# Kernel tuning notes

Hardware: AMD Instinct MI355X
Metric: run time of the kernel (lower is better)

## Reference

```python
import jax, jax.numpy as jnp
import numpy as np

N_DST = 100_000
N_SRC = 200_000
DEG = 16            # fixed avg degree -> E = N_DST*DEG
E = N_DST * DEG
P, K, W = 16, 256, 8  # num_parts, codebook entries, part width; feat_dim = P*W = 128
F_IN = P * W
F_OUT = 128


def setup_inputs() -> dict:
    key = jax.random.key(0)
    k1, k2, k3, k4, k5, k6, k7 = jax.random.split(key, 7)
    codes = jax.random.randint(k1, (N_SRC, P), 0, K, dtype=jnp.int32)
    indices = jax.random.randint(k2, (E,), 0, N_SRC, dtype=jnp.int32)
    indptr = (jnp.arange(N_DST + 1, dtype=jnp.int32) * DEG)
    h_self = jax.random.normal(k3, (N_DST, F_IN), dtype=jnp.float32)
    codebook = jax.random.normal(k4, (P, K, W), dtype=jnp.float32)
    W_neigh = jax.random.normal(k5, (F_OUT, F_IN), dtype=jnp.float32) * (1.0 / np.sqrt(F_IN))
    W_self = jax.random.normal(k6, (F_OUT, F_IN), dtype=jnp.float32) * (1.0 / np.sqrt(F_IN))
    b_self = jax.random.normal(k7, (F_OUT,), dtype=jnp.float32) * 0.01
    return {"codes": codes, "indices": indices, "indptr": indptr, "h_self": h_self,
            "codebook": codebook, "W_neigh": W_neigh, "W_self": W_self, "b_self": b_self}


def reference(codes, indices, indptr, h_self, codebook, W_neigh, W_self, b_self):
    n_dst = indptr.shape[0] - 1
    n_edges = indices.shape[0]
    # --- VQ decompress: codebook[p, codes[n, p]] -> [N_src, P, W] -> [N_src, F_IN]
    feat = codebook[jnp.arange(P)[None, :], codes]          # [N_src, P, W]
    feat = feat.reshape(feat.shape[0], F_IN)                # [N_src, F_IN]
    # --- CSR(CSC) mean SpMM over neighbors
    # dst id of each edge from indptr (jit-safe, static E)
    dst_ids = jnp.searchsorted(indptr, jnp.arange(n_edges, dtype=indptr.dtype), side="right") - 1
    gathered = feat[indices]                                 # [E, F_IN] (irregular gather)
    summed = jax.ops.segment_sum(gathered, dst_ids, num_segments=n_dst)  # [N_dst, F_IN]
    deg = jnp.diff(indptr).astype(summed.dtype)
    h_neigh = summed / jnp.maximum(deg, 1.0)[:, None]        # mean aggregation
    # --- linear combine: fc_neigh(h_neigh) + fc_self(h_self)
    rst = h_neigh @ W_neigh.T + h_self @ W_self.T + b_self[None, :]
    return rst
```

## Files before the change

### kernel.cpp

```cpp
#include <hip/hip_runtime.h>
#include <stdint.h>

constexpr int N_DST = 100000;
constexpr int N_SRC = 200000;
constexpr int DEG   = 16;
constexpr int PP    = 16;
constexpr int KK    = 256;
constexpr int WW    = 8;
constexpr int F_IN  = 128;
constexpr int F_OUT = 128;

constexpr int DT = 64;
constexpr int NT = (N_DST + DT - 1) / DT;
constexpr int LDS_STRIDE = 264;
constexpr int NBLK = 256;

typedef __attribute__((ext_vector_type(8))) short short8;
typedef __attribute__((ext_vector_type(4))) float floatx4;

__device__ __forceinline__ unsigned short f2bf(float f) {
    unsigned int u = __float_as_uint(f);
    unsigned int r = (u + 0x7FFFu + ((u >> 16) & 1u)) >> 16;
    return (unsigned short)r;
}
__device__ __forceinline__ float bf2f(unsigned int bits16) {
    return __uint_as_float(bits16 << 16);
}

__device__ __forceinline__ void gather_loads(
    int d0, int tid, const int* __restrict__ indices,
    const int* __restrict__ codes, const float* __restrict__ h_self,
    int* c, float4* hv)
{
    const int lane = tid & 63;
    const int wv   = tid >> 6;
    const int p    = lane & 15;
    const int sub  = lane >> 4;
    const int d    = d0 + wv * 4 + sub;
    const int dd   = (d < N_DST) ? d : (N_DST - 1);

    int s[16];
    #pragma unroll
    for (int e = 0; e < 16; ++e) s[e] = indices[dd * DEG + e];

    #pragma unroll
    for (int it = 0; it < 2; ++it) {
        const int j  = tid + it * 1024;
        const int dl = j >> 5, kq = j & 31;
        const int dh = d0 + dl;
        hv[it] = make_float4(0.f, 0.f, 0.f, 0.f);
        if (dh < N_DST) hv[it] = ((const float4*)h_self)[(size_t)dh * 32 + kq];
    }

    #pragma unroll
    for (int e = 0; e < 16; ++e) c[e] = codes[s[e] * PP + p];
}

__device__ __forceinline__ void gather_finish(
    int tid, const int* c, const float4* hv,
    const unsigned short* __restrict__ scb,
    unsigned short (*buf)[LDS_STRIDE])
{
    const int lane = tid & 63;
    const int wv   = tid >> 6;
    const int p    = lane & 15;
    const int sub  = lane >> 4;

    float ga[8];
    #pragma unroll
    for (int i = 0; i < 8; ++i) ga[i] = 0.f;
    #pragma unroll
    for (int e = 0; e < 16; ++e) {
        const uint4 q = *(const uint4*)(scb + (((p << 8) | c[e]) << 3));
        ga[0] += bf2f(q.x & 0xFFFFu);
        ga[1] += bf2f(q.x >> 16);
        ga[2] += bf2f(q.y & 0xFFFFu);
        ga[3] += bf2f(q.y >> 16);
        ga[4] += bf2f(q.z & 0xFFFFu);
        ga[5] += bf2f(q.z >> 16);
        ga[6] += bf2f(q.w & 0xFFFFu);
        ga[7] += bf2f(q.w >> 16);
    }

    uint4 o4;
    o4.x = (unsigned int)f2bf(ga[0] * 0.0625f) | ((unsigned int)f2bf(ga[1] * 0.0625f) << 16);
    o4.y = (unsigned int)f2bf(ga[2] * 0.0625f) | ((unsigned int)f2bf(ga[3] * 0.0625f) << 16);
    o4.z = (unsigned int)f2bf(ga[4] * 0.0625f) | ((unsigned int)f2bf(ga[5] * 0.0625f) << 16);
    o4.w = (unsigned int)f2bf(ga[6] * 0.0625f) | ((unsigned int)f2bf(ga[7] * 0.0625f) << 16);
    *(uint4*)&buf[wv * 4 + sub][p * 8] = o4;

    #pragma unroll
    for (int it = 0; it < 2; ++it) {
        const int j  = tid + it * 1024;
        const int dl = j >> 5, kq = j & 31;
        uint2 w;
        w.x = (unsigned int)f2bf(hv[it].x) | ((unsigned int)f2bf(hv[it].y) << 16);
        w.y = (unsigned int)f2bf(hv[it].z) | ((unsigned int)f2bf(hv[it].w) << 16);
        *(uint2*)&buf[dl][128 + kq * 4] = w;
    }
}

__device__ __forceinline__ void mfma_store(
    int d0, int tid, const short8* bfrag, float bs,
    const unsigned short (*buf)[LDS_STRIDE], float* __restrict__ out)
{
    const int wv   = tid >> 6;
    const int lane = tid & 63;
    const int quad = lane >> 4;
    const int r    = lane & 15;
    const int cg   = wv & 7;
    const int rg   = wv >> 3;

    floatx4 acc0 = (floatx4)(0.f);
    floatx4 acc1 = (floatx4)(0.f);
    #pragma unroll
    for (int kt = 0; kt < 8; ++kt) {
        const short8 a0 = *(const short8*)&buf[rg * 32 + r][kt * 32 + quad * 8];
        const short8 a1 = *(const short8*)&buf[rg * 32 + 16 + r][kt * 32 + quad * 8];
        acc0 = __builtin_amdgcn_mfma_f32_16x16x32_bf16(a0, bfrag[kt], acc0, 0, 0, 0);
        acc1 = __builtin_amdgcn_mfma_f32_16x16x32_bf16(a1, bfrag[kt], acc1, 0, 0, 0);
    }
    #pragma unroll
    for (int e = 0; e < 4; ++e) {
        const int da = d0 + rg * 32 + quad * 4 + e;
        if (da < N_DST) out[(size_t)da * F_OUT + cg * 16 + r] = acc0[e] + bs;
    }
    #pragma unroll
    for (int e = 0; e < 4; ++e) {
        const int db = d0 + rg * 32 + 16 + quad * 4 + e;
        if (db < N_DST) out[(size_t)db * F_OUT + cg * 16 + r] = acc1[e] + bs;
    }
}

__global__ __launch_bounds__(1024, 1) void fused_kernel(
    const int* __restrict__ codes, const int* __restrict__ indices,
    const float* __restrict__ codebook, const float* __restrict__ h_self,
    const float* __restrict__ Wn, const float* __restrict__ Ws,
    const float* __restrict__ b_self, float* __restrict__ out)
{
    __shared__ __align__(16) unsigned short scb[PP * KK * WW];
    __shared__ __align__(16) unsigned short hcat[2][DT][LDS_STRIDE];

    const int tid  = threadIdx.x;
    const int wv   = tid >> 6;
    const int lane = tid & 63;
    const int quad = lane >> 4;
    const int r    = lane & 15;

    {
        const float4* cb4 = (const float4*)codebook;
        ushort4* s4 = (ushort4*)scb;
        #pragma unroll
        for (int it = 0; it < 8; ++it) {
            const int i = tid + it * 1024;
            const float4 v = cb4[i];
            ushort4 w;
            w.x = f2bf(v.x); w.y = f2bf(v.y); w.z = f2bf(v.z); w.w = f2bf(v.w);
            s4[i] = w;
        }
    }

    const int cg = wv & 7;
    short8 bfrag[8];
    #pragma unroll
    for (int kt = 0; kt < 8; ++kt) {
        const int o  = cg * 16 + r;
        const int kb = kt * 32 + quad * 8;
        const float* src = (kb < 128) ? (Wn + o * 128 + kb)
                                      : (Ws + o * 128 + (kb - 128));
        union { short8 v; unsigned short u[8]; } f;
        #pragma unroll
        for (int j = 0; j < 8; ++j) f.u[j] = f2bf(src[j]);
        bfrag[kt] = f.v;
    }
    const float bs = b_self[cg * 16 + r];

    __syncthreads();

    const int t0 = (int)(((long long)blockIdx.x * NT) / NBLK);
    const int t1 = (int)(((long long)(blockIdx.x + 1) * NT) / NBLK);

    {
        int c[16]; float4 hv[2];
        gather_loads(t0 * DT, tid, indices, codes, h_self, c, hv);
        gather_finish(tid, c, hv, scb, hcat[0]);
    }

    for (int t = t0; t < t1; ++t) {
        const int cur = (t - t0) & 1;
        __syncthreads();

        int c[16]; float4 hv[2];
        const bool more = (t + 1 < t1);
        if (more) gather_loads((t + 1) * DT, tid, indices, codes, h_self, c, hv);

        mfma_store(t * DT, tid, bfrag, bs, hcat[cur], out);

        if (more) gather_finish(tid, c, hv, scb, hcat[cur ^ 1]);
    }
}

extern "C" void kernel_launch(void* const* d_in, const int* in_sizes, int n_in,
                              void* d_out, int out_size, void* d_ws, size_t ws_size,
                              hipStream_t stream) {
    const int*   codes    = (const int*)d_in[0];
    const int*   indices  = (const int*)d_in[1];
    const float* h_self   = (const float*)d_in[3];
    const float* codebook = (const float*)d_in[4];
    const float* W_neigh  = (const float*)d_in[5];
    const float* W_self   = (const float*)d_in[6];
    const float* b_self   = (const float*)d_in[7];
    float*       out      = (float*)d_out;

    fused_kernel<<<NBLK, 1024, 0, stream>>>(codes, indices, codebook, h_self,
                                            W_neigh, W_self, b_self, out);
}
```

Measured before the change: 165.8 us.

## Move codebook out of LDS to global bf16 and shrink blocks for occupancy

```diff
diff --git a/kernel.cpp b/kernel.cpp
--- a/kernel.cpp
+++ b/kernel.cpp
@@ -10,10 +10,10 @@
 constexpr int F_IN  = 128;
 constexpr int F_OUT = 128;
 
-constexpr int DT = 64;
-constexpr int NT = (N_DST + DT - 1) / DT;
+constexpr int DT   = 32;
+constexpr int NTT  = (N_DST + DT - 1) / DT;
+constexpr int NBLK = 1024;
 constexpr int LDS_STRIDE = 264;
-constexpr int NBLK = 256;
 
 typedef __attribute__((ext_vector_type(8))) short short8;
 typedef __attribute__((ext_vector_type(4))) float floatx4;
@@ -27,6 +27,17 @@
     return __uint_as_float(bits16 << 16);
 }
 
+__global__ void cbconv_kernel(const float* __restrict__ cb,
+                              unsigned short* __restrict__ gcb)
+{
+    const int i = blockIdx.x * 256 + threadIdx.x;
+    const float4 v = ((const float4*)cb)[i];
+    ushort4 w;
+    w.x = f2bf(v.x); w.y = f2bf(v.y); w.z = f2bf(v.z); w.w = f2bf(v.w);
+    ((ushort4*)gcb)[i] = w;
+}
+
+template <bool GCB>
 __device__ __forceinline__ void gather_loads(
     int d0, int tid, const int* __restrict__ indices,
     const int* __restrict__ codes, const float* __restrict__ h_self,
@@ -45,7 +56,7 @@
 
     #pragma unroll
     for (int it = 0; it < 2; ++it) {
-        const int j  = tid + it * 1024;
+        const int j  = tid + it * 512;
         const int dl = j >> 5, kq = j & 31;
         const int dh = d0 + dl;
         hv[it] = make_float4(0.f, 0.f, 0.f, 0.f);
@@ -56,9 +67,10 @@
     for (int e = 0; e < 16; ++e) c[e] = codes[s[e] * PP + p];
 }
 
+template <bool GCB>
 __device__ __forceinline__ void gather_finish(
     int tid, const int* c, const float4* hv,
-    const unsigned short* __restrict__ scb,
+    const unsigned short* __restrict__ gcb, const float* __restrict__ cbf,
     unsigned short (*buf)[LDS_STRIDE])
 {
     const int lane = tid & 63;
@@ -69,17 +81,25 @@
     float ga[8];
     #pragma unroll
     for (int i = 0; i < 8; ++i) ga[i] = 0.f;
+
     #pragma unroll
     for (int e = 0; e < 16; ++e) {
-        const uint4 q = *(const uint4*)(scb + (((p << 8) | c[e]) << 3));
-        ga[0] += bf2f(q.x & 0xFFFFu);
-        ga[1] += bf2f(q.x >> 16);
-        ga[2] += bf2f(q.y & 0xFFFFu);
-        ga[3] += bf2f(q.y >> 16);
-        ga[4] += bf2f(q.z & 0xFFFFu);
-        ga[5] += bf2f(q.z >> 16);
-        ga[6] += bf2f(q.w & 0xFFFFu);
-        ga[7] += bf2f(q.w >> 16);
+        if (GCB) {
+            const uint4 q = *(const uint4*)(gcb + (((p << 8) | c[e]) << 3));
+            ga[0] += bf2f(q.x & 0xFFFFu);
+            ga[1] += bf2f(q.x >> 16);
+            ga[2] += bf2f(q.y & 0xFFFFu);
+            ga[3] += bf2f(q.y >> 16);
+            ga[4] += bf2f(q.z & 0xFFFFu);
+            ga[5] += bf2f(q.z >> 16);
+            ga[6] += bf2f(q.w & 0xFFFFu);
+            ga[7] += bf2f(q.w >> 16);
+        } else {
+            const float4 q0 = *(const float4*)(cbf + (((p << 8) | c[e]) << 3));
+            const float4 q1 = *(const float4*)(cbf + (((p << 8) | c[e]) << 3) + 4);
+            ga[0] += q0.x; ga[1] += q0.y; ga[2] += q0.z; ga[3] += q0.w;
+            ga[4] += q1.x; ga[5] += q1.y; ga[6] += q1.z; ga[7] += q1.w;
+        }
     }
 
     uint4 o4;
@@ -91,7 +111,7 @@
 
     #pragma unroll
     for (int it = 0; it < 2; ++it) {
-        const int j  = tid + it * 1024;
+        const int j  = tid + it * 512;
         const int dl = j >> 5, kq = j & 31;
         uint2 w;
         w.x = (unsigned int)f2bf(hv[it].x) | ((unsigned int)f2bf(hv[it].y) << 16);
@@ -108,37 +128,36 @@
     const int lane = tid & 63;
     const int quad = lane >> 4;
     const int r    = lane & 15;
-    const int cg   = wv & 7;
-    const int rg   = wv >> 3;
 
     floatx4 acc0 = (floatx4)(0.f);
     floatx4 acc1 = (floatx4)(0.f);
     #pragma unroll
     for (int kt = 0; kt < 8; ++kt) {
-        const short8 a0 = *(const short8*)&buf[rg * 32 + r][kt * 32 + quad * 8];
-        const short8 a1 = *(const short8*)&buf[rg * 32 + 16 + r][kt * 32 + quad * 8];
+        const short8 a0 = *(const short8*)&buf[r][kt * 32 + quad * 8];
+        const short8 a1 = *(const short8*)&buf[16 + r][kt * 32 + quad * 8];
         acc0 = __builtin_amdgcn_mfma_f32_16x16x32_bf16(a0, bfrag[kt], acc0, 0, 0, 0);
         acc1 = __builtin_amdgcn_mfma_f32_16x16x32_bf16(a1, bfrag[kt], acc1, 0, 0, 0);
     }
     #pragma unroll
     for (int e = 0; e < 4; ++e) {
-        const int da = d0 + rg * 32 + quad * 4 + e;
-        if (da < N_DST) out[(size_t)da * F_OUT + cg * 16 + r] = acc0[e] + bs;
+        const int da = d0 + quad * 4 + e;
+        if (da < N_DST) out[(size_t)da * F_OUT + wv * 16 + r] = acc0[e] + bs;
     }
     #pragma unroll
     for (int e = 0; e < 4; ++e) {
-        const int db = d0 + rg * 32 + 16 + quad * 4 + e;
-        if (db < N_DST) out[(size_t)db * F_OUT + cg * 16 + r] = acc1[e] + bs;
-    }
-}
-
-__global__ __launch_bounds__(1024, 1) void fused_kernel(
+        const int db = d0 + 16 + quad * 4 + e;
+        if (db < N_DST) out[(size_t)db * F_OUT + wv * 16 + r] = acc1[e] + bs;
+    }
+}
+
+template <bool GCB>
+__global__ __launch_bounds__(512) void fused_kernel(
     const int* __restrict__ codes, const int* __restrict__ indices,
-    const float* __restrict__ codebook, const float* __restrict__ h_self,
+    const unsigned short* __restrict__ gcb, const float* __restrict__ cbf,
+    const float* __restrict__ h_self,
     const float* __restrict__ Wn, const float* __restrict__ Ws,
     const float* __restrict__ b_self, float* __restrict__ out)
 {
-    __shared__ __align__(16) unsigned short scb[PP * KK * WW];
     __shared__ __align__(16) unsigned short hcat[2][DT][LDS_STRIDE];
 
     const int tid  = threadIdx.x;
@@ -147,24 +166,10 @@
     const int quad = lane >> 4;
     const int r    = lane & 15;
 
-    {
-        const float4* cb4 = (const float4*)codebook;
-        ushort4* s4 = (ushort4*)scb;
-        #pragma unroll
-        for (int it = 0; it < 8; ++it) {
-            const int i = tid + it * 1024;
-            const float4 v = cb4[i];
-            ushort4 w;
-            w.x = f2bf(v.x); w.y = f2bf(v.y); w.z = f2bf(v.z); w.w = f2bf(v.w);
-            s4[i] = w;
-        }
-    }
-
-    const int cg = wv & 7;
     short8 bfrag[8];
     #pragma unroll
     for (int kt = 0; kt < 8; ++kt) {
-        const int o  = cg * 16 + r;
+        const int o  = wv * 16 + r;
         const int kb = kt * 32 + quad * 8;
         const float* src = (kb < 128) ? (Wn + o * 128 + kb)
                                       : (Ws + o * 128 + (kb - 128));
@@ -173,17 +178,16 @@
         for (int j = 0; j < 8; ++j) f.u[j] = f2bf(src[j]);
         bfrag[kt] = f.v;
     }
-    const float bs = b_self[cg * 16 + r];
-
-    __syncthreads();
-
-    const int t0 = (int)(((long long)blockIdx.x * NT) / NBLK);
-    const int t1 = (int)(((long long)(blockIdx.x + 1) * NT) / NBLK);
+    const float bs = b_self[wv * 16 + r];
+
+    const int t0 = (int)(((long long)blockIdx.x * NTT) / NBLK);
+    const int t1 = (int)(((long long)(blockIdx.x + 1) * NTT) / NBLK);
+    if (t0 >= t1) return;
 
     {
         int c[16]; float4 hv[2];
-        gather_loads(t0 * DT, tid, indices, codes, h_self, c, hv);
-        gather_finish(tid, c, hv, scb, hcat[0]);
+        gather_loads<GCB>(t0 * DT, tid, indices, codes, h_self, c, hv);
+        gather_finish<GCB>(tid, c, hv, gcb, cbf, hcat[0]);
     }
 
     for (int t = t0; t < t1; ++t) {
@@ -192,11 +196,11 @@
 
         int c[16]; float4 hv[2];
         const bool more = (t + 1 < t1);
-        if (more) gather_loads((t + 1) * DT, tid, indices, codes, h_self, c, hv);
+        if (more) gather_loads<GCB>((t + 1) * DT, tid, indices, codes, h_self, c, hv);
 
         mfma_store(t * DT, tid, bfrag, bs, hcat[cur], out);
 
-        if (more) gather_finish(tid, c, hv, scb, hcat[cur ^ 1]);
+        if (more) gather_finish<GCB>(tid, c, hv, gcb, cbf, hcat[cur ^ 1]);
     }
 }
 
@@ -212,6 +216,14 @@
     const float* b_self   = (const float*)d_in[7];
     float*       out      = (float*)d_out;
 
-    fused_kernel<<<NBLK, 1024, 0, stream>>>(codes, indices, codebook, h_self,
-                                            W_neigh, W_self, b_self, out);
-}
+    if (ws_size >= (size_t)(PP * KK * WW * 2)) {
+        unsigned short* gcb = (unsigned short*)d_ws;
+        cbconv_kernel<<<32, 256, 0, stream>>>(codebook, gcb);
+        fused_kernel<true><<<NBLK, 512, 0, stream>>>(
+            codes, indices, gcb, codebook, h_self, W_neigh, W_self, b_self, out);
+    } else {
+        fused_kernel<false><<<NBLK, 512, 0, stream>>>(
+            codes, indices, (const unsigned short*)nullptr, codebook, h_self,
+            W_neigh, W_self, b_self, out);
+    }
+}
```

Result: slower. 216.1 us (+30.4%).
